# Kernel tuning notes

Hardware: AMD Instinct MI355X
Metric: run time of the kernel (lower is better)

## Reference

```python
import jax, jax.numpy as jnp
import numpy as np

H = 8192  # hidden width; structure = [42, H, H, 8]


def setup_inputs() -> dict:
    key = jax.random.key(0)
    ks = jax.random.split(key, 6)
    # Connect-4 board: 42 cells with values 0 (empty), 1, 2 (players)
    state = jax.random.randint(ks[0], (42,), 0, 3).astype(jnp.float32)
    state = state.at[0].set(0.0)  # guarantee at least one legal column
    s = 0.02
    W1 = jax.random.normal(ks[1], (42, H), jnp.float32) * s
    b1 = jnp.zeros((H,), jnp.float32)
    W2 = jax.random.normal(ks[2], (H, H), jnp.float32) * s
    b2 = jnp.zeros((H,), jnp.float32)
    W3 = jax.random.normal(ks[3], (H, 8), jnp.float32) * s
    b3 = jnp.zeros((8,), jnp.float32)
    return {"state": state, "W1": W1, "b1": b1, "W2": W2, "b2": b2,
            "W3": W3, "b3": b3}


def reference(state, W1, b1, W2, b2, W3, b3):
    x = state.reshape(1, 42)
    x = jax.nn.relu(x @ W1 + b1)          # [1, H]
    x = jax.nn.relu(x @ W2 + b2)          # [1, H]
    pen = x @ W3 + b3                      # [1, 8] = 7 move logits + value
    value = pen[:, -1]                     # [1]
    # mask(state): column i legal iff top-row cell state[i] == 0
    legal = state[:7] == 0                 # [7] bool
    logits = pen[0, :7]                    # [7]
    masked = jnp.where(legal, logits, -jnp.inf)
    p = jax.nn.softmax(masked)             # softmax over legal entries only
    # scatter reduced distribution back into fixed [7,1] slots
    distribution = jnp.where(legal, p, 0.0).reshape(7, 1)
    return (value, distribution)
```

## Files before the change

### kernel.cpp

```cpp
#include <hip/hip_runtime.h>
#include <math.h>

#define H 8192
#define NSPLIT 64
#define NSEG 8
#define SEGCOLS 1024

typedef float floatx4 __attribute__((ext_vector_type(4)));

#define WS_VALS 0
#define WS_ROWS 8192
#define WS_CNT 16384
#define WS_PEN 16392
#define WS_PARTIAL 16400

__global__ void k1_h1(const float* __restrict__ state,
                      const float* __restrict__ W1,
                      const float* __restrict__ b1,
                      float* __restrict__ vals,
                      int* __restrict__ rows,
                      int* __restrict__ cnt,
                      float* __restrict__ pen) {
    __shared__ float sv[SEGCOLS];
    __shared__ int   sr[SEGCOLS];
    __shared__ int   scnt;
    int tid = threadIdx.x;
    if (tid == 0) scnt = 0;
    if (blockIdx.x == 0 && tid < 8) pen[tid] = 0.0f;
    __syncthreads();

    int j = blockIdx.x * SEGCOLS + tid * 4;
    float4 acc = *(const float4*)(b1 + j);
    #pragma unroll 6
    for (int i = 0; i < 42; ++i) {
        float s = state[i];
        float4 w = *(const float4*)(W1 + (size_t)i * H + j);
        acc.x = fmaf(s, w.x, acc.x);
        acc.y = fmaf(s, w.y, acc.y);
        acc.z = fmaf(s, w.z, acc.z);
        acc.w = fmaf(s, w.w, acc.w);
    }
    float v[4] = { fmaxf(acc.x, 0.f), fmaxf(acc.y, 0.f),
                   fmaxf(acc.z, 0.f), fmaxf(acc.w, 0.f) };
    #pragma unroll
    for (int c = 0; c < 4; ++c) {
        if (v[c] > 0.0f) {
            int p = atomicAdd(&scnt, 1);
            sv[p] = v[c];
            sr[p] = j + c;
        }
    }
    __syncthreads();
    int n = scnt;
    if (tid == 0) cnt[blockIdx.x] = n;
    int base = blockIdx.x * SEGCOLS;
    for (int p = tid; p < n; p += blockDim.x) {
        vals[base + p] = sv[p];
        rows[base + p] = sr[p];
    }
}

__global__ __launch_bounds__(256) void k2_partial(
        const float* __restrict__ W2,
        const float* __restrict__ vals,
        const int* __restrict__ rows,
        const int* __restrict__ cnt,
        float* __restrict__ partial) {
    int j = blockIdx.x * SEGCOLS + threadIdx.x * 4;

    int c[NSEG], pre[NSEG + 1];
    pre[0] = 0;
    #pragma unroll
    for (int b = 0; b < NSEG; ++b) { c[b] = cnt[b]; pre[b + 1] = pre[b] + c[b]; }
    int total = pre[NSEG];
    int chunk = (total + NSPLIT - 1) / NSPLIT;
    int glo = blockIdx.y * chunk;
    int ghi = min(glo + chunk, total);

    float4 acc = make_float4(0.f, 0.f, 0.f, 0.f);
    #pragma unroll
    for (int b = 0; b < NSEG; ++b) {
        int lo = max(glo, pre[b]);
        int hi = min(ghi, pre[b] + c[b]);
        int off = b * SEGCOLS - pre[b];
        #pragma unroll 8
        for (int p = lo; p < hi; ++p) {
            float s = vals[off + p];
            int   r = rows[off + p];
            const floatx4* wp = (const floatx4*)(W2 + (size_t)r * H + j);
            floatx4 w = __builtin_nontemporal_load(wp);
            acc.x = fmaf(s, w.x, acc.x);
            acc.y = fmaf(s, w.y, acc.y);
            acc.z = fmaf(s, w.z, acc.z);
            acc.w = fmaf(s, w.w, acc.w);
        }
    }
    *(float4*)(partial + (size_t)blockIdx.y * H + j) = acc;
}

__global__ void k3_reduce(const float* __restrict__ partial,
                          const float* __restrict__ b2,
                          const float* __restrict__ W3,
                          float* __restrict__ pen) {
    int j = blockIdx.x * blockDim.x + threadIdx.x;
    float acc = b2[j];
    #pragma unroll 8
    for (int s = 0; s < NSPLIT; ++s)
        acc += __builtin_nontemporal_load(partial + (size_t)s * H + j);
    float h = fmaxf(acc, 0.0f);

    float4 w0 = *(const float4*)(W3 + (size_t)j * 8);
    float4 w1 = *(const float4*)(W3 + (size_t)j * 8 + 4);
    float a[8] = { h * w0.x, h * w0.y, h * w0.z, h * w0.w,
                   h * w1.x, h * w1.y, h * w1.z, h * w1.w };

    #pragma unroll
    for (int off = 32; off > 0; off >>= 1) {
        #pragma unroll
        for (int k = 0; k < 8; ++k) a[k] += __shfl_down(a[k], off);
    }
    if ((threadIdx.x & 63) == 0) {
        #pragma unroll
        for (int k = 0; k < 8; ++k) atomicAdd(&pen[k], a[k]);
    }
}

__global__ void k4_final(const float* __restrict__ pen,
                         const float* __restrict__ b3,
                         const float* __restrict__ state,
                         float* __restrict__ out) {
    if (threadIdx.x == 0) {
        float p8[8];
        #pragma unroll
        for (int k = 0; k < 8; ++k) p8[k] = pen[k] + b3[k];
        out[0] = p8[7];
        bool legal[7];
        float m = -INFINITY;
        for (int i = 0; i < 7; ++i) {
            legal[i] = (state[i] == 0.0f);
            if (legal[i] && p8[i] > m) m = p8[i];
        }
        float e[7], sum = 0.0f;
        for (int i = 0; i < 7; ++i) {
            e[i] = legal[i] ? expf(p8[i] - m) : 0.0f;
            sum += e[i];
        }
        float inv = 1.0f / sum;
        for (int i = 0; i < 7; ++i) out[1 + i] = e[i] * inv;
    }
}

extern "C" void kernel_launch(void* const* d_in, const int* in_sizes, int n_in,
                              void* d_out, int out_size, void* d_ws, size_t ws_size,
                              hipStream_t stream) {
    const float* state = (const float*)d_in[0];
    const float* W1    = (const float*)d_in[1];
    const float* b1    = (const float*)d_in[2];
    const float* W2    = (const float*)d_in[3];
    const float* b2    = (const float*)d_in[4];
    const float* W3    = (const float*)d_in[5];
    const float* b3    = (const float*)d_in[6];
    float* out = (float*)d_out;

    float* ws      = (float*)d_ws;
    float* vals    = ws + WS_VALS;
    int*   rows    = (int*)(ws + WS_ROWS);
    int*   cnt     = (int*)(ws + WS_CNT);
    float* pen     = ws + WS_PEN;
    float* partial = ws + WS_PARTIAL;

    hipLaunchKernelGGL(k1_h1, dim3(NSEG), dim3(256), 0, stream,
                       state, W1, b1, vals, rows, cnt, pen);
    hipLaunchKernelGGL(k2_partial, dim3(H / SEGCOLS, NSPLIT), dim3(256), 0, stream,
                       W2, vals, rows, cnt, partial);
    hipLaunchKernelGGL(k3_reduce, dim3(H / 256), dim3(256), 0, stream,
                       partial, b2, W3, pen);
    hipLaunchKernelGGL(k4_final, dim3(1), dim3(64), 0, stream,
                       pen, b3, state, out);
}
```

Measured before the change: 352.2 us.

## Fuse final softmax into reduce, stage sparse rows in LDS, widen layer-1 grid

Layer 1 now runs on 32 blocks of 64 threads instead of 8 blocks of 256, and stores each active row as a premultiplied offset. The layer-2 kernel first gathers its chunk of (value, row offset) pairs into shared memory, then streams W2 with a single flat loop instead of a nested per-segment loop. The separate final softmax kernel is folded into the reduce kernel: the last block to finish, found through an atomic counter, computes the outputs. This saves a launch and cuts index work in the hot loop, at the cost of a 128-entry cap on chunk size and a last-block fence pattern.

```diff
diff --git a/kernel.cpp b/kernel.cpp
--- a/kernel.cpp
+++ b/kernel.cpp
@@ -3,35 +3,41 @@
 
 #define H 8192
 #define NSPLIT 64
-#define NSEG 8
-#define SEGCOLS 1024
+#define NSEG 32
+#define SEGSZ 256
+#define XSTRIPE 1024
 
 typedef float floatx4 __attribute__((ext_vector_type(4)));
 
 #define WS_VALS 0
 #define WS_ROWS 8192
 #define WS_CNT 16384
-#define WS_PEN 16392
-#define WS_PARTIAL 16400
-
-__global__ void k1_h1(const float* __restrict__ state,
+#define WS_PEN 16416
+#define WS_CTR 16424
+#define WS_PARTIAL 16432
+
+__global__ __launch_bounds__(64) void k1_h1(const float* __restrict__ state,
                       const float* __restrict__ W1,
                       const float* __restrict__ b1,
                       float* __restrict__ vals,
                       int* __restrict__ rows,
                       int* __restrict__ cnt,
-                      float* __restrict__ pen) {
-    __shared__ float sv[SEGCOLS];
-    __shared__ int   sr[SEGCOLS];
+                      float* __restrict__ pen,
+                      int* __restrict__ ctr) {
+    __shared__ float sv[SEGSZ];
+    __shared__ int   sr[SEGSZ];
     __shared__ int   scnt;
     int tid = threadIdx.x;
     if (tid == 0) scnt = 0;
-    if (blockIdx.x == 0 && tid < 8) pen[tid] = 0.0f;
-    __syncthreads();
-
-    int j = blockIdx.x * SEGCOLS + tid * 4;
+    if (blockIdx.x == 0) {
+        if (tid < 8) pen[tid] = 0.0f;
+        if (tid == 8) *ctr = 0;
+    }
+    __syncthreads();
+
+    int j = blockIdx.x * SEGSZ + tid * 4;
     float4 acc = *(const float4*)(b1 + j);
-    #pragma unroll 6
+    #pragma unroll
     for (int i = 0; i < 42; ++i) {
         float s = state[i];
         float4 w = *(const float4*)(W1 + (size_t)i * H + j);
@@ -47,14 +53,14 @@
         if (v[c] > 0.0f) {
             int p = atomicAdd(&scnt, 1);
             sv[p] = v[c];
-            sr[p] = j + c;
+            sr[p] = (j + c) * H;
         }
     }
     __syncthreads();
     int n = scnt;
     if (tid == 0) cnt[blockIdx.x] = n;
-    int base = blockIdx.x * SEGCOLS;
-    for (int p = tid; p < n; p += blockDim.x) {
+    int base = blockIdx.x * SEGSZ;
+    for (int p = tid; p < n; p += 64) {
         vals[base + p] = sv[p];
         rows[base + p] = sr[p];
     }
@@ -66,43 +72,58 @@
         const int* __restrict__ rows,
         const int* __restrict__ cnt,
         float* __restrict__ partial) {
-    int j = blockIdx.x * SEGCOLS + threadIdx.x * 4;
-
-    int c[NSEG], pre[NSEG + 1];
+    __shared__ float sval[128];
+    __shared__ int   srow[128];
+    int tid = threadIdx.x;
+
+    int pre[NSEG + 1];
     pre[0] = 0;
     #pragma unroll
-    for (int b = 0; b < NSEG; ++b) { c[b] = cnt[b]; pre[b + 1] = pre[b] + c[b]; }
+    for (int b = 0; b < NSEG; ++b) pre[b + 1] = pre[b] + cnt[b];
     int total = pre[NSEG];
     int chunk = (total + NSPLIT - 1) / NSPLIT;
     int glo = blockIdx.y * chunk;
     int ghi = min(glo + chunk, total);
-
-    float4 acc = make_float4(0.f, 0.f, 0.f, 0.f);
-    #pragma unroll
-    for (int b = 0; b < NSEG; ++b) {
-        int lo = max(glo, pre[b]);
-        int hi = min(ghi, pre[b] + c[b]);
-        int off = b * SEGCOLS - pre[b];
-        #pragma unroll 8
-        for (int p = lo; p < hi; ++p) {
-            float s = vals[off + p];
-            int   r = rows[off + p];
-            const floatx4* wp = (const floatx4*)(W2 + (size_t)r * H + j);
-            floatx4 w = __builtin_nontemporal_load(wp);
-            acc.x = fmaf(s, w.x, acc.x);
-            acc.y = fmaf(s, w.y, acc.y);
-            acc.z = fmaf(s, w.z, acc.z);
-            acc.w = fmaf(s, w.w, acc.w);
+    int n = (ghi > glo) ? (ghi - glo) : 0;
+
+    if (tid < n) {
+        int p = glo + tid;
+        int src = 0;
+        #pragma unroll
+        for (int b = 0; b < NSEG; ++b) {
+            if (p >= pre[b] && p < pre[b + 1]) src = p - pre[b] + b * SEGSZ;
         }
-    }
-    *(float4*)(partial + (size_t)blockIdx.y * H + j) = acc;
-}
-
-__global__ void k3_reduce(const float* __restrict__ partial,
+        sval[tid] = vals[src];
+        srow[tid] = rows[src];
+    }
+    __syncthreads();
+
+    int j = blockIdx.x * XSTRIPE + tid * 4;
+    const float* wbase = W2 + j;
+    floatx4 acc = (floatx4)0.0f;
+    #pragma unroll 8
+    for (int i = 0; i < n; ++i) {
+        float s  = sval[i];
+        int roff = srow[i];
+        floatx4 w = __builtin_nontemporal_load((const floatx4*)(wbase + roff));
+        acc.x = fmaf(s, w.x, acc.x);
+        acc.y = fmaf(s, w.y, acc.y);
+        acc.z = fmaf(s, w.z, acc.z);
+        acc.w = fmaf(s, w.w, acc.w);
+    }
+    *(floatx4*)(partial + (size_t)blockIdx.y * H + j) = acc;
+}
+
+__global__ __launch_bounds__(256) void k3_reduce(const float* __restrict__ partial,
                           const float* __restrict__ b2,
                           const float* __restrict__ W3,
-                          float* __restrict__ pen) {
-    int j = blockIdx.x * blockDim.x + threadIdx.x;
+                          float* __restrict__ pen,
+                          int* __restrict__ ctr,
+                          const float* __restrict__ b3,
+                          const float* __restrict__ state,
+                          float* __restrict__ out) {
+    int tid = threadIdx.x;
+    int j = blockIdx.x * 256 + tid;
     float acc = b2[j];
     #pragma unroll 8
     for (int s = 0; s < NSPLIT; ++s)
@@ -119,34 +140,34 @@
         #pragma unroll
         for (int k = 0; k < 8; ++k) a[k] += __shfl_down(a[k], off);
     }
-    if ((threadIdx.x & 63) == 0) {
+    if ((tid & 63) == 0) {
         #pragma unroll
         for (int k = 0; k < 8; ++k) atomicAdd(&pen[k], a[k]);
     }
-}
-
-__global__ void k4_final(const float* __restrict__ pen,
-                         const float* __restrict__ b3,
-                         const float* __restrict__ state,
-                         float* __restrict__ out) {
-    if (threadIdx.x == 0) {
-        float p8[8];
-        #pragma unroll
-        for (int k = 0; k < 8; ++k) p8[k] = pen[k] + b3[k];
-        out[0] = p8[7];
-        bool legal[7];
-        float m = -INFINITY;
-        for (int i = 0; i < 7; ++i) {
-            legal[i] = (state[i] == 0.0f);
-            if (legal[i] && p8[i] > m) m = p8[i];
+
+    __syncthreads();
+    if (tid == 0) {
+        __threadfence();
+        if (atomicAdd(ctr, 1) == (int)gridDim.x - 1) {
+            float p8[8];
+            #pragma unroll
+            for (int k = 0; k < 8; ++k)
+                p8[k] = atomicAdd(&pen[k], 0.0f) + b3[k];
+            out[0] = p8[7];
+            bool legal[7];
+            float m = -INFINITY;
+            for (int i = 0; i < 7; ++i) {
+                legal[i] = (state[i] == 0.0f);
+                if (legal[i] && p8[i] > m) m = p8[i];
+            }
+            float e[7], sum = 0.0f;
+            for (int i = 0; i < 7; ++i) {
+                e[i] = legal[i] ? expf(p8[i] - m) : 0.0f;
+                sum += e[i];
+            }
+            float inv = 1.0f / sum;
+            for (int i = 0; i < 7; ++i) out[1 + i] = e[i] * inv;
         }
-        float e[7], sum = 0.0f;
-        for (int i = 0; i < 7; ++i) {
-            e[i] = legal[i] ? expf(p8[i] - m) : 0.0f;
-            sum += e[i];
-        }
-        float inv = 1.0f / sum;
-        for (int i = 0; i < 7; ++i) out[1 + i] = e[i] * inv;
     }
 }
 
@@ -167,14 +188,13 @@
     int*   rows    = (int*)(ws + WS_ROWS);
     int*   cnt     = (int*)(ws + WS_CNT);
     float* pen     = ws + WS_PEN;
+    int*   ctr     = (int*)(ws + WS_CTR);
     float* partial = ws + WS_PARTIAL;
 
-    hipLaunchKernelGGL(k1_h1, dim3(NSEG), dim3(256), 0, stream,
-                       state, W1, b1, vals, rows, cnt, pen);
-    hipLaunchKernelGGL(k2_partial, dim3(H / SEGCOLS, NSPLIT), dim3(256), 0, stream,
+    hipLaunchKernelGGL(k1_h1, dim3(NSEG), dim3(64), 0, stream,
+                       state, W1, b1, vals, rows, cnt, pen, ctr);
+    hipLaunchKernelGGL(k2_partial, dim3(H / XSTRIPE, NSPLIT), dim3(256), 0, stream,
                        W2, vals, rows, cnt, partial);
     hipLaunchKernelGGL(k3_reduce, dim3(H / 256), dim3(256), 0, stream,
-                       partial, b2, W3, pen);
-    hipLaunchKernelGGL(k4_final, dim3(1), dim3(64), 0, stream,
-                       pen, b3, state, out);
-}
+                       partial, b2, W3, pen, ctr, b3, state, out);
+}
```

Result: no change. 346.0 us (-1.7%).
